# Optimization experiments

Measured on AMD Instinct MI355X. Metric: run time of the kernel, lower is better.

The kernel has to match this reference:

```python
import jax, jax.numpy as jnp
import numpy as np
import math

L, H, DH, D, M, V, S, B = 4, 12, 64, 768, 3072, 32000, 1024, 2


def _xavier(k, shape):
    fan_in, fan_out = shape[-2], shape[-1]
    std = math.sqrt(2.0 / (fan_in + fan_out))
    return (jax.random.normal(k, shape, jnp.float32) * std).astype(jnp.float32)


def setup_inputs() -> dict:
    key = jax.random.key(0)
    ks = jax.random.split(key, 20)
    inp = {}
    inp['x'] = jax.random.randint(ks[0], (B, S), 0, V)
    inp['E_w'] = _xavier(ks[1], (V, D))
    inp['P_w'] = _xavier(ks[2], (S, D))
    inp['ln1_w'] = jnp.ones((L, D), jnp.float32)
    inp['ln1_b'] = jnp.zeros((L, D), jnp.float32)
    inp['Q_w'] = _xavier(ks[3], (L, H, D, DH))
    inp['Q_b'] = 0.02 * jax.random.normal(ks[4], (L, H, DH), jnp.float32)
    inp['K_w'] = _xavier(ks[5], (L, H, D, DH))
    inp['K_b'] = 0.02 * jax.random.normal(ks[6], (L, H, DH), jnp.float32)
    inp['V_w'] = _xavier(ks[7], (L, H, D, DH))
    inp['V_b'] = 0.02 * jax.random.normal(ks[8], (L, H, DH), jnp.float32)
    inp['O_w'] = _xavier(ks[9], (L, H, DH, D))
    inp['O_b'] = 0.02 * jax.random.normal(ks[10], (L, D), jnp.float32)
    inp['ln2_w'] = jnp.ones((L, D), jnp.float32)
    inp['ln2_b'] = jnp.zeros((L, D), jnp.float32)
    inp['In_w'] = _xavier(ks[11], (L, D, M))
    inp['In_b'] = 0.02 * jax.random.normal(ks[12], (L, M), jnp.float32)
    inp['Out_w'] = _xavier(ks[13], (L, M, D))
    inp['Out_b'] = 0.02 * jax.random.normal(ks[14], (L, D), jnp.float32)
    inp['lnf_w'] = jnp.ones((D,), jnp.float32)
    inp['lnf_b'] = jnp.zeros((D,), jnp.float32)
    inp['U_w'] = _xavier(ks[15], (D, V))
    inp['U_b'] = jnp.zeros((V,), jnp.float32)
    return inp


def _layernorm(x, w, b):
    # torch x.std() is unbiased (ddof=1)
    mu = x.mean(-1, keepdims=True)
    sd = jnp.std(x, axis=-1, keepdims=True, ddof=1)
    return w * ((x - mu) / sd) + b


def reference(x, E_w, P_w, ln1_w, ln1_b, Q_w, Q_b, K_w, K_b, V_w, V_b, O_w, O_b,
              ln2_w, ln2_b, In_w, In_b, Out_w, Out_b, lnf_w, lnf_b, U_w, U_b):
    seq = x.shape[1]
    res = E_w[x] + P_w[:seq][None, :, :]  # [B,S,D]
    mask = jnp.triu(jnp.ones((seq, seq), bool), k=1)  # future positions
    scale = 1.0 / math.sqrt(DH)
    for l in range(L):
        h = _layernorm(res, ln1_w[l], ln1_b[l])
        q = jnp.einsum('bsd,hde->bshe', h, Q_w[l]) + Q_b[l]
        k = jnp.einsum('bsd,hde->bshe', h, K_w[l]) + K_b[l]
        logits = jnp.einsum('bqhe,bkhe->bhqk', q, k) * scale
        logits = jnp.where(mask, -100000.0, logits)  # masked_fill_
        scores = jax.nn.softmax(logits, axis=-1)
        v = jnp.einsum('bsd,hde->bshe', h, V_w[l]) + V_b[l]
        attn = jnp.einsum('bhqk,bkhe->bqhe', scores, v)
        o = jnp.einsum('bqhe,hed->bqd', attn, O_w[l]) + O_b[l]
        res_attn = res + o
        h2 = _layernorm(res_attn, ln2_w[l], ln2_b[l])
        m = jax.nn.gelu(jnp.einsum('bsd,dm->bsm', h2, In_w[l]) + In_b[l], approximate=False)
        m = jnp.einsum('bsm,md->bsd', m, Out_w[l]) + Out_b[l]
        res = res + res_attn + m  # note: double residual, as in source
    res = _layernorm(res, lnf_w, lnf_b)
    return jnp.einsum('bsd,dv->bsv', res, U_w) + U_b
```

## Files before the change

kernel.cpp:

```cpp
#include <hip/hip_runtime.h>

using uint = unsigned int;
using u16  = unsigned short;
using ll   = long long;

constexpr int cL = 4, cH = 12, cDH = 64, cD = 768, cM = 3072, cV = 32000, cS = 1024, cB = 2;
constexpr int cT  = cB * cS;
constexpr int cBH = cB * cH;
constexpr int cQKV = 3 * cD;

using bf16x8 = __bf16 __attribute__((ext_vector_type(8)));
using f32x4  = float  __attribute__((ext_vector_type(4)));

__device__ __forceinline__ float b2f(u16 u) {
    union { uint i; float f; } v; v.i = ((uint)u) << 16; return v.f;
}
__device__ __forceinline__ u16 f2b(float f) {
    union { float f; uint i; } v; v.f = f;
    uint u = v.i;
    return (u16)((u + 0x7fffu + ((u >> 16) & 1u)) >> 16);
}
__device__ __forceinline__ float inp(const void* p, ll idx, int md) {
    return md ? b2f(((const u16*)p)[idx]) : ((const float*)p)[idx];
}
__device__ __forceinline__ float wave_sum(float v) {
    #pragma unroll
    for (int m = 32; m; m >>= 1) v += __shfl_xor(v, m);
    return v;
}
__device__ __forceinline__ float wave_max(float v) {
    #pragma unroll
    for (int m = 32; m; m >>= 1) v = fmaxf(v, __shfl_xor(v, m));
    return v;
}
__device__ __forceinline__ void gload16(const u16* g, u16* l) {
    __builtin_amdgcn_global_load_lds(
        (const __attribute__((address_space(1))) uint*)g,
        (__attribute__((address_space(3))) uint*)l,
        16, 0, 0);
}

__global__ void detect_k(const uint* __restrict__ e, int* __restrict__ flag)
{
    const int l = threadIdx.x;
    int hits = 0;
    #pragma unroll
    for (int i = 0; i < 4; ++i) {
        uint w  = e[l * 4 + i];
        uint ex = (w >> 7) & 0xffu;
        hits += (ex >= 100u && ex <= 126u) ? 1 : 0;
    }
    float s = wave_sum((float)hits);
    if (l == 0) *flag = (s >= 128.f) ? 1 : 0;
}

__global__ __launch_bounds__(256)
void packbias_k(const void* __restrict__ Qb, const void* __restrict__ Kb,
                const void* __restrict__ Vb, float* __restrict__ out,
                const int* __restrict__ modeflag)
{
    const int md = *modeflag;
    const int i = blockIdx.x * 256 + threadIdx.x;
    const int l = i / cQKV, c = i % cQKV;
    float v;
    if (c < cD)           v = inp(Qb, (ll)l * cD + c, md);
    else if (c < 2 * cD)  v = inp(Kb, (ll)l * cD + c - cD, md);
    else                  v = inp(Vb, (ll)l * cD + c - 2 * cD, md);
    out[i] = v;
}

template<int BM, int BN, int WGM, int WGN, int OUTK, bool GELU,
         bool COLMAJ, bool CSKIP, bool CK, int BIASK, bool XCDS = false>
__global__ __launch_bounds__(256)
void gemm_bt(const u16* __restrict__ A, int lda, ll offAo, ll offAi,
             const u16* __restrict__ Bt, int ldb, ll offBo, ll offBi,
             void* __restrict__ Cv, int ldc, ll offCo, ll offCi,
             int HB, int K,
             const void* __restrict__ bias, ll bias_off, float scale,
             const float* __restrict__ r1, const float* __restrict__ r2,
             const int* __restrict__ modeflag)
{
    constexpr int MF = BM / WGM / 16;
    constexpr int NF = BN / WGN / 16;
    static_assert(BM % (WGM * 16) == 0 && BN % (WGN * 16) == 0, "tile/wave mismatch");
    static_assert(WGM * WGN == 4, "4 waves");
    __shared__ __align__(16) u16 sA[BM * 64];
    __shared__ __align__(16) u16 sB[BN * 64];

    int rowTile, colTile;
    if constexpr (CSKIP) {
        const int bi = blockIdx.x;
        int r = (int)((sqrtf(8.f * bi + 1.f) - 1.f) * 0.5f);
        while ((r + 1) * (r + 2) / 2 <= bi) ++r;
        while (r * (r + 1) / 2 > bi) --r;
        rowTile = r * BM;
        colTile = (bi - r * (r + 1) / 2) * BN;
    } else if constexpr (XCDS) {
        const int nwg = gridDim.x * gridDim.y;
        const int lin = blockIdx.y * gridDim.x + blockIdx.x;
        const int q8 = nwg >> 3, r8 = nwg & 7;
        const int xcd = lin & 7, idx = lin >> 3;
        const int n_  = (xcd < r8 ? xcd * (q8 + 1) : r8 * (q8 + 1) + (xcd - r8) * q8) + idx;
        rowTile = (n_ % gridDim.x) * BM;
        colTile = (n_ / gridDim.x) * BN;
    } else {
        rowTile = (COLMAJ ? blockIdx.x : blockIdx.y) * BM;
        colTile = (COLMAJ ? blockIdx.y : blockIdx.x) * BN;
    }

    const int md = *modeflag;
    const int z = blockIdx.z;
    const ll zo = z / HB, zi = z % HB;
    const u16* Ab = A + zo * offAo + zi * offAi;
    const u16* Bb = Bt + zo * offBo + zi * offBi;

    const int tid  = threadIdx.x;
    const int lane = tid & 63, wid = tid >> 6;
    const int wr = wid / WGN, wc = wid % WGN;
    const int lr = lane >> 3;
    const int lc8s = (((lane & 7) ^ lr) << 3);

    f32x4 zero = {0.f, 0.f, 0.f, 0.f};
    f32x4 acc[MF][NF];
    #pragma unroll
    for (int m = 0; m < MF; ++m)
        #pragma unroll
        for (int n = 0; n < NF; ++n) acc[m][n] = zero;

    const int nkt = CK ? ((rowTile + BM) >> 6) : (K >> 6);
    for (int kt = 0; kt < nkt; ++kt) {
        const int k0 = kt << 6;
        #pragma unroll
        for (int i = 0; i < BM / 32; ++i) {
            int c = i * 4 + wid;
            gload16(Ab + (size_t)(rowTile + c * 8 + lr) * lda + k0 + lc8s, &sA[c * 512]);
        }
        #pragma unroll
        for (int i = 0; i < BN / 32; ++i) {
            int c = i * 4 + wid;
            gload16(Bb + (size_t)(colTile + c * 8 + lr) * ldb + k0 + lc8s, &sB[c * 512]);
        }
        asm volatile("s_waitcnt vmcnt(0)" ::: "memory");
        __syncthreads();
        #pragma unroll
        for (int kk = 0; kk < 2; ++kk) {
            const int g = kk * 4 + (lane >> 4);
            bf16x8 af[MF], bfv[NF];
            #pragma unroll
            for (int m = 0; m < MF; ++m) {
                const int row = wr * (BM / WGM) + m * 16 + (lane & 15);
                af[m] = *(const bf16x8*)&sA[row * 64 + ((g ^ (row & 7)) << 3)];
            }
            #pragma unroll
            for (int n = 0; n < NF; ++n) {
                const int row = wc * (BN / WGN) + n * 16 + (lane & 15);
                bfv[n] = *(const bf16x8*)&sB[row * 64 + ((g ^ (row & 7)) << 3)];
            }
            #pragma unroll
            for (int m = 0; m < MF; ++m)
                #pragma unroll
                for (int n = 0; n < NF; ++n)
                    acc[m][n] = __builtin_amdgcn_mfma_f32_16x16x32_bf16(af[m], bfv[n], acc[m][n], 0, 0, 0);
        }
        __syncthreads();
    }

    const ll offC = zo * offCo + zi * offCi;
    #pragma unroll
    for (int m = 0; m < MF; ++m) {
        #pragma unroll
        for (int n = 0; n < NF; ++n) {
            const int col = colTile + wc * (BN / WGN) + n * 16 + (lane & 15);
            float bvv = 0.f;
            if constexpr (BIASK == 1) bvv = inp(bias, bias_off + col, md);
            if constexpr (BIASK == 2) bvv = ((const float*)bias)[bias_off + col];
            #pragma unroll
            for (int r = 0; r < 4; ++r) {
                const int row = rowTile + wr * (BM / WGM) + m * 16 + ((lane >> 4) << 2) + r;
                float xv = acc[m][n][r] * scale + bvv;
                if constexpr (GELU) xv = 0.5f * xv * (1.f + erff(xv * 0.70710678118654752f));
                const size_t idx = (size_t)row * ldc + col;
                if (r1) xv += r1[idx];
                if (r2) xv += r2[idx];
                if constexpr (OUTK == 1)      ((u16*)Cv)[offC + idx] = f2b(xv);
                else if constexpr (OUTK == 0) ((float*)Cv)[offC + idx] = xv;
                else {
                    if (md) ((u16*)Cv)[offC + idx] = f2b(xv);
                    else    ((float*)Cv)[offC + idx] = xv;
                }
            }
        }
    }
}

__global__ __launch_bounds__(256)
void transpose_k(const void* __restrict__ in, u16* __restrict__ out,
                 int R, int C, int ins, int outs,
                 ll base, ll iStride, ll oStride,
                 const int* __restrict__ modeflag)
{
    __shared__ u16 tile[32][33];
    const int md = *modeflag;
    const int z = blockIdx.z;
    const ll ioff = base + (ll)z * iStride;
    u16* op = out + (ll)z * oStride;
    const int tx = threadIdx.x & 31, ty = threadIdx.x >> 5;
    const int c0 = blockIdx.x * 32, r0 = blockIdx.y * 32;
    #pragma unroll
    for (int i = 0; i < 32; i += 8) {
        int r = r0 + ty + i, c = c0 + tx;
        if (r < R && c < C) tile[ty + i][tx] = f2b(inp(in, ioff + (ll)r * ins + c, md));
    }
    __syncthreads();
    #pragma unroll
    for (int i = 0; i < 32; i += 8) {
        int c = c0 + ty + i, r = r0 + tx;
        if (c < C && r < R) op[(size_t)c * outs + r] = tile[tx][ty + i];
    }
}

__global__ __launch_bounds__(256)
void transw_k(const void* __restrict__ Qw, const void* __restrict__ Kw,
              const void* __restrict__ Vw, const void* __restrict__ Ow,
              const void* __restrict__ Inw, const void* __restrict__ Outw,
              u16* __restrict__ WqkvT, u16* __restrict__ WoT,
              u16* __restrict__ WinT, u16* __restrict__ WoutT,
              int l, const int* __restrict__ modeflag)
{
    __shared__ u16 tile[32][33];
    const int md = *modeflag;
    const int b = blockIdx.x;
    const void* in; u16* out; int ins, outs, tx_, ty_; ll ibase;
    if (b < 1728) {
        const int seg = b / 576, rem = b % 576, hd = rem / 48, tt = rem % 48;
        in = seg == 0 ? Qw : (seg == 1 ? Kw : Vw);
        ibase = (ll)l * cH * cD * cDH + (ll)hd * cD * cDH;
        out = WqkvT + (ll)seg * cD * cD + (ll)hd * cDH * cD;
        ins = cDH; outs = cD; tx_ = tt % 2; ty_ = tt / 2;
    } else if (b < 2304) {
        const int tt = b - 1728;
        in = Ow; ibase = (ll)l * cD * cD; out = WoT;
        ins = cD; outs = cD; tx_ = tt % 24; ty_ = tt / 24;
    } else if (b < 4608) {
        const int tt = b - 2304;
        in = Inw; ibase = (ll)l * cD * cM; out = WinT;
        ins = cM; outs = cD; tx_ = tt % 96; ty_ = tt / 96;
    } else {
        const int tt = b - 4608;
        in = Outw; ibase = (ll)l * cM * cD; out = WoutT;
        ins = cD; outs = cM; tx_ = tt % 24; ty_ = tt / 24;
    }
    const int tx = threadIdx.x & 31, ty = threadIdx.x >> 5;
    const int c0 = tx_ * 32, r0 = ty_ * 32;
    #pragma unroll
    for (int i = 0; i < 32; i += 8)
        tile[ty + i][tx] = f2b(inp(in, ibase + (ll)(r0 + ty + i) * ins + c0 + tx, md));
    __syncthreads();
    #pragma unroll
    for (int i = 0; i < 32; i += 8)
        out[(size_t)(c0 + ty + i) * outs + (r0 + tx)] = tile[tx][ty + i];
}

__global__ __launch_bounds__(256)
void transpose_b_k(const u16* __restrict__ in, u16* __restrict__ out,
                   int R, int C, int ins, int outs,
                   ll iOo, ll iOi, ll oOo, ll oOi, int HB)
{
    __shared__ u16 tile[32][33];
    const int z = blockIdx.z;
    const u16* ip = in  + (ll)(z / HB) * iOo + (ll)(z % HB) * iOi;
    u16*       op = out + (ll)(z / HB) * oOo + (ll)(z % HB) * oOi;
    const int tx = threadIdx.x & 31, ty = threadIdx.x >> 5;
    const int c0 = blockIdx.x * 32, r0 = blockIdx.y * 32;
    #pragma unroll
    for (int i = 0; i < 32; i += 8) {
        int r = r0 + ty + i, c = c0 + tx;
        if (r < R && c < C) tile[ty + i][tx] = ip[(size_t)r * ins + c];
    }
    __syncthreads();
    #pragma unroll
    for (int i = 0; i < 32; i += 8) {
        int c = c0 + ty + i, r = r0 + tx;
        if (c < C && r < R) op[(size_t)c * outs + r] = tile[tx][ty + i];
    }
}

__global__ __launch_bounds__(192)
void embed_k(const int* __restrict__ x, const void* __restrict__ E,
             const void* __restrict__ P, float* __restrict__ res,
             const int* __restrict__ modeflag)
{
    const int md = *modeflag;
    const int tok = blockIdx.x, t = threadIdx.x;
    const int s = tok & (cS - 1);
    const ll  eb = (ll)x[tok] * cD, pb = (ll)s * cD;
    float4 o;
    o.x = inp(E, eb + t * 4 + 0, md) + inp(P, pb + t * 4 + 0, md);
    o.y = inp(E, eb + t * 4 + 1, md) + inp(P, pb + t * 4 + 1, md);
    o.z = inp(E, eb + t * 4 + 2, md) + inp(P, pb + t * 4 + 2, md);
    o.w = inp(E, eb + t * 4 + 3, md) + inp(P, pb + t * 4 + 3, md);
    ((float4*)(res + (size_t)tok * cD))[t] = o;
}

__global__ __launch_bounds__(192)
void ln_k(const float* __restrict__ in, const void* __restrict__ w,
          const void* __restrict__ b, ll wb_off, u16* __restrict__ out,
          const int* __restrict__ modeflag)
{
    __shared__ float sm[8];
    const int md = *modeflag;
    const int row = blockIdx.x, t = threadIdx.x;
    const float4 x = ((const float4*)(in + (size_t)row * cD))[t];
    float s = wave_sum(x.x + x.y + x.z + x.w);
    const int lane = t & 63, wv = t >> 6;
    if (!lane) sm[wv] = s;
    __syncthreads();
    const float mu = (sm[0] + sm[1] + sm[2]) * (1.f / (float)cD);
    const float dx = x.x - mu, dy = x.y - mu, dz = x.z - mu, dw = x.w - mu;
    float ss = wave_sum(dx * dx + dy * dy + dz * dz + dw * dw);
    if (!lane) sm[4 + wv] = ss;
    __syncthreads();
    const float var = (sm[4] + sm[5] + sm[6]) * (1.f / (float)(cD - 1));
    const float rs  = 1.f / sqrtf(var);
    const ll o4 = wb_off + (ll)t * 4;
    ushort4 o;
    o.x = f2b(inp(w, o4 + 0, md) * (dx * rs) + inp(b, o4 + 0, md));
    o.y = f2b(inp(w, o4 + 1, md) * (dy * rs) + inp(b, o4 + 1, md));
    o.z = f2b(inp(w, o4 + 2, md) * (dz * rs) + inp(b, o4 + 2, md));
    o.w = f2b(inp(w, o4 + 3, md) * (dw * rs) + inp(b, o4 + 3, md));
    ((ushort4*)(out + (size_t)row * cD))[t] = o;
}

__global__ __launch_bounds__(256)
void softmax4_k(u16* __restrict__ p)
{
    const int row = blockIdx.x * 4 + (threadIdx.x >> 6);
    const int q = row & (cS - 1);
    u16* pr = p + (size_t)row * cS;
    const int lane = threadIdx.x & 63;

    ushort4 v[4];
    float xs[16];
    float mx = -3.4e38f;
    #pragma unroll
    for (int c = 0; c < 4; ++c) {
        const int j0 = (lane + c * 64) * 4;
        v[c] = make_ushort4(0, 0, 0, 0);
        if (j0 <= q) v[c] = ((const ushort4*)pr)[lane + c * 64];
        xs[c * 4 + 0] = (j0 + 0 <= q) ? b2f(v[c].x) : -100000.f;
        xs[c * 4 + 1] = (j0 + 1 <= q) ? b2f(v[c].y) : -100000.f;
        xs[c * 4 + 2] = (j0 + 2 <= q) ? b2f(v[c].z) : -100000.f;
        xs[c * 4 + 3] = (j0 + 3 <= q) ? b2f(v[c].w) : -100000.f;
        mx = fmaxf(mx, fmaxf(fmaxf(xs[c * 4], xs[c * 4 + 1]), fmaxf(xs[c * 4 + 2], xs[c * 4 + 3])));
    }
    mx = wave_max(mx);
    float sum = 0.f;
    #pragma unroll
    for (int j = 0; j < 16; ++j) {
        xs[j] = expf(xs[j] - mx);
        sum += xs[j];
    }
    sum = wave_sum(sum);
    const float inv = 1.f / sum;
    #pragma unroll
    for (int c = 0; c < 4; ++c) {
        ushort4 o;
        o.x = f2b(xs[c * 4 + 0] * inv);
        o.y = f2b(xs[c * 4 + 1] * inv);
        o.z = f2b(xs[c * 4 + 2] * inv);
        o.w = f2b(xs[c * 4 + 3] * inv);
        ((ushort4*)pr)[lane + c * 64] = o;
    }
}

extern "C" void kernel_launch(void* const* d_in, const int* in_sizes, int n_in,
                              void* d_out, int out_size, void* d_ws, size_t ws_size,
                              hipStream_t stream)
{
    (void)in_sizes; (void)n_in; (void)out_size;
    const int*  x     = (const int*)d_in[0];
    const void* E_w   = d_in[1];
    const void* P_w   = d_in[2];
    const void* ln1_w = d_in[3];
    const void* ln1_b = d_in[4];
    const void* Q_w   = d_in[5];
    const void* Q_b   = d_in[6];
    const void* K_w   = d_in[7];
    const void* K_b   = d_in[8];
    const void* V_w   = d_in[9];
    const void* V_b   = d_in[10];
    const void* O_w   = d_in[11];
    const void* O_b   = d_in[12];
    const void* ln2_w = d_in[13];
    const void* ln2_b = d_in[14];
    const void* In_w  = d_in[15];
    const void* In_b  = d_in[16];
    const void* Out_w = d_in[17];
    const void* Out_b = d_in[18];
    const void* lnf_w = d_in[19];
    const void* lnf_b = d_in[20];
    const void* U_w   = d_in[21];
    const void* U_b   = d_in[22];

    char* wp = (char*)d_ws;
    auto carve = [&](size_t bytes) { char* r = wp; wp += (bytes + 255) & ~(size_t)255; return r; };
    int*   modeflag = (int*)carve(256);
    float* biasQKV  = (float*)carve((size_t)cL * cQKV * 4);
    float* res   = (float*)carve((size_t)cT * cD * 4);
    float* resat = (float*)carve((size_t)cT * cD * 4);
    u16* h     = (u16*)carve((size_t)cT * cD * 2);
    u16* attnb = (u16*)carve((size_t)cT * cD * 2);
    u16* vt    = (u16*)carve((size_t)cT * cD * 2);
    u16* qkv   = (u16*)carve((size_t)cT * cM * 2);
    u16* mlpb  = qkv;
    u16* WqkvT = (u16*)carve((size_t)cQKV * cD * 2);
    u16* WoT   = (u16*)carve((size_t)cD * cD * 2);
    u16* WinT  = (u16*)carve((size_t)cD * cM * 2);
    u16* WoutT = (u16*)carve((size_t)cD * cM * 2);
    u16* pbuf  = (u16*)carve((size_t)cBH * cS * cS * 2);
    u16* WuT   = pbuf;

    if (ws_size && (size_t)(wp - (char*)d_ws) > ws_size) return;

    detect_k<<<1, 64, 0, stream>>>((const uint*)E_w, modeflag);
    packbias_k<<<(cL * cQKV) / 256, 256, 0, stream>>>(Q_b, K_b, V_b, biasQKV, modeflag);
    embed_k<<<cT, 192, 0, stream>>>(x, E_w, P_w, res, modeflag);

    for (int l = 0; l < cL; ++l) {
        transw_k<<<6912, 256, 0, stream>>>(Q_w, K_w, V_w, O_w, In_w, Out_w,
                                           WqkvT, WoT, WinT, WoutT, l, modeflag);

        ln_k<<<cT, 192, 0, stream>>>(res, ln1_w, ln1_b, (ll)l * cD, h, modeflag);

        gemm_bt<64, 128, 1, 4, 1, false, true, false, false, 2>
            <<<dim3(cT / 64, cQKV / 128, 1), 256, 0, stream>>>(
            h, cD, 0, 0, WqkvT, cD, 0, 0, qkv, cQKV, 0, 0, 1, cD,
            biasQKV, (ll)l * cQKV, 1.f, nullptr, nullptr, modeflag);

        transpose_b_k<<<dim3(2, cS / 32, cBH), 256, 0, stream>>>(
            qkv + 2 * cD, vt, cS, cDH, cQKV, cS,
            (ll)cS * cQKV, cDH, (ll)cH * cDH * cS, (ll)cDH * cS, cH);

        gemm_bt<128, 128, 2, 2, 1, false, false, true, false, 0>
            <<<dim3(36, 1, cBH), 256, 0, stream>>>(
            qkv, cQKV, (ll)cS * cQKV, cDH,
            qkv + cD, cQKV, (ll)cS * cQKV, cDH,
            pbuf, cS, (ll)cH * cS * cS, (ll)cS * cS,
            cH, cDH, nullptr, 0, 0.125f, nullptr, nullptr, modeflag);

        softmax4_k<<<cBH * cS / 4, 256, 0, stream>>>(pbuf);

        gemm_bt<64, 64, 2, 2, 1, false, false, false, true, 0>
            <<<dim3(1, 16, cBH), 256, 0, stream>>>(
            pbuf, cS, (ll)cH * cS * cS, (ll)cS * cS,
            vt, cS, (ll)cH * cDH * cS, (ll)cDH * cS,
            attnb, cD, (ll)cS * cD, cDH,
            cH, cS, nullptr, 0, 1.f, nullptr, nullptr, modeflag);

        gemm_bt<128, 128, 2, 2, 0, false, true, false, false, 1>
            <<<dim3(cT / 128, cD / 128, 1), 256, 0, stream>>>(
            attnb, cD, 0, 0, WoT, cD, 0, 0, resat, cD, 0, 0, 1, cD,
            O_b, (ll)l * cD, 1.f, res, nullptr, modeflag);

        ln_k<<<cT, 192, 0, stream>>>(resat, ln2_w, ln2_b, (ll)l * cD, h, modeflag);

        gemm_bt<64, 128, 1, 4, 1, true, true, false, false, 1>
            <<<dim3(cT / 64, cM / 128, 1), 256, 0, stream>>>(
            h, cD, 0, 0, WinT, cD, 0, 0, mlpb, cM, 0, 0, 1, cD,
            In_b, (ll)l * cM, 1.f, nullptr, nullptr, modeflag);

        gemm_bt<64, 64, 2, 2, 0, false, true, false, false, 1>
            <<<dim3(cT / 64, cD / 64, 1), 256, 0, stream>>>(
            mlpb, cM, 0, 0, WoutT, cM, 0, 0, res, cD, 0, 0, 1, cM,
            Out_b, (ll)l * cD, 1.f, res, resat, modeflag);
    }

    transpose_k<<<dim3(cV / 32, cD / 32, 1), 256, 0, stream>>>(
        U_w, WuT, cD, cV, cV, cD, 0, 0, 0, modeflag);
    ln_k<<<cT, 192, 0, stream>>>(res, lnf_w, lnf_b, 0, h, modeflag);
    gemm_bt<64, 128, 1, 4, 2, false, true, false, false, 1, true>
        <<<dim3(cT / 64, cV / 128, 1), 256, 0, stream>>>(
        h, cD, 0, 0, WuT, cD, 0, 0, d_out, cV, 0, 0, 1, cD,
        U_b, 0, 1.f, nullptr, nullptr, modeflag);
}
```

Before: 1.018 ms.

## Fuse ln1 into weight-transpose launch and retune several GEMM tile shapes

Merges the first layernorm of each layer into the weight-transpose kernel as extra blocks, which removes one launch per layer and lets the two run concurrently. Changes the attention logits GEMM from 128x128 to 64x64 tiles (more causal-triangle blocks), the O-projection from 128x128 to 64x64 tiles, and the unembedding GEMM from 64x128 to 128x128 tiles with a changed template flag. The goal is better occupancy and wave balance on the smaller GEMMs and more reuse on the large vocab GEMM. The trade-offs are more blocks with less reuse per block on the smaller GEMMs, and the altered template flag on the final GEMM may change its epilogue path.

```diff
diff --git a/kernel.cpp b/kernel.cpp
--- a/kernel.cpp
+++ b/kernel.cpp
@@ -220,16 +220,47 @@
 }
 
 __global__ __launch_bounds__(256)
-void transw_k(const void* __restrict__ Qw, const void* __restrict__ Kw,
-              const void* __restrict__ Vw, const void* __restrict__ Ow,
-              const void* __restrict__ Inw, const void* __restrict__ Outw,
-              u16* __restrict__ WqkvT, u16* __restrict__ WoT,
-              u16* __restrict__ WinT, u16* __restrict__ WoutT,
-              int l, const int* __restrict__ modeflag)
+void transln_k(const void* __restrict__ Qw, const void* __restrict__ Kw,
+               const void* __restrict__ Vw, const void* __restrict__ Ow,
+               const void* __restrict__ Inw, const void* __restrict__ Outw,
+               u16* __restrict__ WqkvT, u16* __restrict__ WoT,
+               u16* __restrict__ WinT, u16* __restrict__ WoutT,
+               const float* __restrict__ res, const void* __restrict__ lnw,
+               const void* __restrict__ lnb, ll wb_off, u16* __restrict__ hout,
+               int l, const int* __restrict__ modeflag)
 {
     __shared__ u16 tile[32][33];
+    __shared__ float sm[8];
     const int md = *modeflag;
     const int b = blockIdx.x;
+
+    if (b >= 6912) {
+        const int row = b - 6912, t = threadIdx.x;
+        float4 x = {0.f, 0.f, 0.f, 0.f};
+        if (t < 192) x = ((const float4*)(res + (size_t)row * cD))[t];
+        float s = wave_sum(x.x + x.y + x.z + x.w);
+        const int lane = t & 63, wv = t >> 6;
+        if (!lane) sm[wv] = s;
+        __syncthreads();
+        const float mu = (sm[0] + sm[1] + sm[2]) * (1.f / (float)cD);
+        const float dx = x.x - mu, dy = x.y - mu, dz = x.z - mu, dw = x.w - mu;
+        float ss = wave_sum(dx * dx + dy * dy + dz * dz + dw * dw);
+        if (!lane) sm[4 + wv] = ss;
+        __syncthreads();
+        const float var = (sm[4] + sm[5] + sm[6]) * (1.f / (float)(cD - 1));
+        const float rs  = 1.f / sqrtf(var);
+        if (t < 192) {
+            const ll o4 = wb_off + (ll)t * 4;
+            ushort4 o;
+            o.x = f2b(inp(lnw, o4 + 0, md) * (dx * rs) + inp(lnb, o4 + 0, md));
+            o.y = f2b(inp(lnw, o4 + 1, md) * (dy * rs) + inp(lnb, o4 + 1, md));
+            o.z = f2b(inp(lnw, o4 + 2, md) * (dz * rs) + inp(lnb, o4 + 2, md));
+            o.w = f2b(inp(lnw, o4 + 3, md) * (dw * rs) + inp(lnb, o4 + 3, md));
+            ((ushort4*)(hout + (size_t)row * cD))[t] = o;
+        }
+        return;
+    }
+
     const void* in; u16* out; int ins, outs, tx_, ty_; ll ibase;
     if (b < 1728) {
         const int seg = b / 576, rem = b % 576, hd = rem / 48, tt = rem % 48;
@@ -427,10 +458,9 @@
     embed_k<<<cT, 192, 0, stream>>>(x, E_w, P_w, res, modeflag);
 
     for (int l = 0; l < cL; ++l) {
-        transw_k<<<6912, 256, 0, stream>>>(Q_w, K_w, V_w, O_w, In_w, Out_w,
-                                           WqkvT, WoT, WinT, WoutT, l, modeflag);
-
-        ln_k<<<cT, 192, 0, stream>>>(res, ln1_w, ln1_b, (ll)l * cD, h, modeflag);
+        transln_k<<<6912 + cT, 256, 0, stream>>>(
+            Q_w, K_w, V_w, O_w, In_w, Out_w, WqkvT, WoT, WinT, WoutT,
+            res, ln1_w, ln1_b, (ll)l * cD, h, l, modeflag);
 
         gemm_bt<64, 128, 1, 4, 1, false, true, false, false, 2>
             <<<dim3(cT / 64, cQKV / 128, 1), 256, 0, stream>>>(
@@ -441,8 +471,8 @@
             qkv + 2 * cD, vt, cS, cDH, cQKV, cS,
             (ll)cS * cQKV, cDH, (ll)cH * cDH * cS, (ll)cDH * cS, cH);
 
-        gemm_bt<128, 128, 2, 2, 1, false, false, true, false, 0>
-            <<<dim3(36, 1, cBH), 256, 0, stream>>>(
+        gemm_bt<64, 64, 2, 2, 1, false, false, true, false, 0>
+            <<<dim3(136, 1, cBH), 256, 0, stream>>>(
             qkv, cQKV, (ll)cS * cQKV, cDH,
             qkv + cD, cQKV, (ll)cS * cQKV, cDH,
             pbuf, cS, (ll)cH * cS * cS, (ll)cS * cS,
@@ -457,8 +487,8 @@
             attnb, cD, (ll)cS * cD, cDH,
             cH, cS, nullptr, 0, 1.f, nullptr, nullptr, modeflag);
 
-        gemm_bt<128, 128, 2, 2, 0, false, true, false, false, 1>
-            <<<dim3(cT / 128, cD / 128, 1), 256, 0, stream>>>(
+        gemm_bt<64, 64, 2, 2, 0, false, true, false, false, 1>
+            <<<dim3(cT / 64, cD / 64, 1), 256, 0, stream>>>(
             attnb, cD, 0, 0, WoT, cD, 0, 0, resat, cD, 0, 0, 1, cD,
             O_b, (ll)l * cD, 1.f, res, nullptr, modeflag);
 
@@ -478,8 +508,8 @@
     transpose_k<<<dim3(cV / 32, cD / 32, 1), 256, 0, stream>>>(
         U_w, WuT, cD, cV, cV, cD, 0, 0, 0, modeflag);
     ln_k<<<cT, 192, 0, stream>>>(res, lnf_w, lnf_b, 0, h, modeflag);
-    gemm_bt<64, 128, 1, 4, 2, false, true, false, false, 1, true>
-        <<<dim3(cT / 64, cV / 128, 1), 256, 0, stream>>>(
+    gemm_bt<128, 128, 2, 2, 2, false, false, false, false, 1, true>
+        <<<dim3(cT / 128, cV / 128, 1), 256, 0, stream>>>(
         h, cD, 0, 0, WuT, cD, 0, 0, d_out, cV, 0, 0, 1, cD,
         U_b, 0, 1.f, nullptr, nullptr, modeflag);
 }
```

Result: faster. 928.0 us (-8.9%).
